# Kernel optimization log

Hardware: AMD Instinct MI355X
Metric: run time of the kernel (lower is better)

The kernel has to match this reference:

```python
import jax, jax.numpy as jnp
import numpy as np
from jax import lax

GAMMA = 1.0
BIG = 1e8  # matches the torch init value 100000000.0


def setup_inputs() -> dict:
    key = jax.random.key(0)
    k1, k2 = jax.random.split(key)
    B, n, m, d = 256, 256, 256, 32
    x = jax.random.normal(k1, (B, n, d), dtype=jnp.float32)
    y = jax.random.normal(k2, (B, m, d), dtype=jnp.float32)
    return {"x": x, "y": y}


def _soft_dtw(x, y, gamma):
    B, n, d = x.shape
    m = y.shape[1]
    # squared euclidean distances, (B, n, m); GEMM form avoids the (B,n,m,d) blowup
    x2 = jnp.sum(x * x, axis=-1)
    y2 = jnp.sum(y * y, axis=-1)
    dist = x2[:, :, None] + y2[:, None, :] - 2.0 * jnp.einsum('bnd,bmd->bnm', x, y)
    dist = jnp.maximum(dist, 0.0)  # cdist(p=2)**2 is nonnegative

    def softmin3(a, b, c):
        s = jnp.stack([a, b, c], axis=0)
        return -gamma * jax.nn.logsumexp(-s / gamma, axis=0)

    big_col = jnp.full((B,), BIG, dtype=x.dtype)

    def row_step(prev_row, d_row):
        # prev_row: (B, m+1) = D[i-1, :];  d_row: (B, m) = dist[:, i-1, :]
        def col_step(cur, inp):
            # cur: (B,) = D[i, j-1]; inp: (dist[i-1,j-1], D[i-1,j], D[i-1,j-1])
            dij, up, diag = inp
            new = dij + softmin3(up, cur, diag)
            return new, new
        xs = (d_row.T, prev_row[:, 1:].T, prev_row[:, :-1].T)  # each (m, B)
        _, vals = lax.scan(col_step, big_col, xs)  # vals: (m, B)
        new_row = jnp.concatenate([big_col[:, None], vals.T], axis=1)  # (B, m+1)
        return new_row, None

    init_row = jnp.concatenate(
        [jnp.zeros((B, 1), x.dtype), jnp.full((B, m), BIG, dtype=x.dtype)], axis=1)
    final_row, _ = lax.scan(row_step, init_row, jnp.swapaxes(dist, 0, 1))  # scan over n rows
    return jnp.mean(final_row[:, m])


def reference(x, y):
    return _soft_dtw(x, y, GAMMA)
```

## Files before the change

### kernel.cpp

```cpp
#include <hip/hip_runtime.h>

#define BIG 1e8f
#define LN2 0.69314718f
#define LOG2E 1.44269504f
#define M2L -2.8853900818f

#define RSLOT 112
#define DRB 1040

#define OFF_XH   116480
#define OFF_X2S  132864
#define OFF_Y2S  133888
#define OFF_RDY  134912
#define OFF_PRG  134976
#define LDS_BYTES 135040

typedef _Float16 half8 __attribute__((ext_vector_type(8)));
typedef _Float16 half2_t __attribute__((ext_vector_type(2)));
typedef float f32x4 __attribute__((ext_vector_type(4)));

__device__ __forceinline__ float exp2g(float x) {
#if __has_builtin(__builtin_amdgcn_exp2f)
    return __builtin_amdgcn_exp2f(x);
#else
    return exp2f(x);
#endif
}
__device__ __forceinline__ float log2g(float x) {
#if __has_builtin(__builtin_amdgcn_logf)
    return __builtin_amdgcn_logf(x);
#else
    return log2f(x);
#endif
}

__device__ __forceinline__ half2_t pkrtz(float a, float b) {
    return __builtin_bit_cast(half2_t, __builtin_amdgcn_cvt_pkrtz(a, b));
}

__device__ __forceinline__ float shfl_up1(float v, float oldv) {
    int r = __builtin_amdgcn_update_dpp(
        __builtin_bit_cast(int, oldv), __builtin_bit_cast(int, v),
        0x138 , 0xf, 0xf, false);
    return __builtin_bit_cast(float, r);
}

__device__ __forceinline__ void dec2(unsigned int w, float& a, float& b) {
    half2_t h = __builtin_bit_cast(half2_t, w);
    a = (float)h[0];
    b = (float)h[1];
}

__device__ __forceinline__ void cell3(float Mu, float Su, float Mg, float Sg,
                                      float Ml, float Sl, float dd,
                                      float& Mo, float& So) {
    const float mu = fminf(fminf(Mu, Mg), Ml);
    const float eu = exp2g(mu - Mu);
    const float eg = exp2g(mu - Mg);
    const float el = exp2g(mu - Ml);
    So = fmaf(Su, eu, fmaf(Sg, eg, Sl * el));
    Mo = dd + mu;
}

#define MASKW0 0x7BFF7BFFu
#define MASKW1 0x70007000u
#define MASKW2 0x60006000u
#define MASKW3 0x50005000u

__global__ __launch_bounds__(128, 1) void sdtw_kernel(
    const float* __restrict__ x, const float* __restrict__ y,
    float* __restrict__ out) {
    extern __shared__ __align__(16) char smem[];
    unsigned char* band = (unsigned char*)smem;
    _Float16* xh = (_Float16*)(smem + OFF_XH);
    float* x2sL = (float*)(smem + OFF_X2S);
    float* y2sL = (float*)(smem + OFF_Y2S);
    volatile int* rdy = (volatile int*)(smem + OFF_RDY);
    volatile int* prg = (volatile int*)(smem + OFF_PRG);

    const int tid = threadIdx.x;
    const int b = blockIdx.x;
    const float* xb = x + (size_t)b * 8192;
    const float* yb = y + (size_t)b * 8192;

#pragma unroll
    for (int rr = 0; rr < 2; rr++) {
        const int r = tid + rr * 128;
        const float4* px = (const float4*)(xb + r * 32);
        union { _Float16 h[32]; half8 v[4]; } uc;
        float s2 = 0.f;
#pragma unroll
        for (int q = 0; q < 8; q++) {
            float4 f = px[q];
            s2 += f.x * f.x + f.y * f.y + f.z * f.z + f.w * f.w;
            uc.h[4 * q + 0] = (_Float16)f.x;
            uc.h[4 * q + 1] = (_Float16)f.y;
            uc.h[4 * q + 2] = (_Float16)f.z;
            uc.h[4 * q + 3] = (_Float16)f.w;
        }
        half8* dst = (half8*)&xh[r * 32];
#pragma unroll
        for (int q = 0; q < 4; q++) dst[q] = uc.v[q];
        x2sL[r] = s2 * LOG2E;

        const float4* py = (const float4*)(yb + r * 32);
        float t2 = 0.f;
#pragma unroll
        for (int q = 0; q < 8; q++) {
            float4 f = py[q];
            t2 += f.x * f.x + f.y * f.y + f.z * f.z + f.w * f.w;
        }
        y2sL[r] = t2 * LOG2E;
    }
    if (tid < 16) rdy[tid] = 0;
    if (tid == 16) *prg = 0;
    __syncthreads();

    if (tid >= 64) {
        const int lane = tid - 64;
        const int qd = lane >> 4, xr = lane & 15;

        half8 yfrag[16];
        float yvL[16];
#pragma unroll
        for (int ci = 0; ci < 16; ci++) {
            const float* yp = yb + (ci * 16 + xr) * 32 + qd * 8;
            float4 f0 = *(const float4*)yp;
            float4 f1 = *(const float4*)(yp + 4);
            half8 v;
            v[0] = (_Float16)f0.x; v[1] = (_Float16)f0.y;
            v[2] = (_Float16)f0.z; v[3] = (_Float16)f0.w;
            v[4] = (_Float16)f1.x; v[5] = (_Float16)f1.y;
            v[6] = (_Float16)f1.z; v[7] = (_Float16)f1.w;
            yfrag[ci] = v;
            yvL[ci] = y2sL[ci * 16 + xr];
        }

        for (int sg = 0; sg < 16; sg++) {
            if (sg >= 6) {
                const int need = 8 * sg - 40;
                while (*prg < need) {}
            }
            const half8 xf = *(const half8*)&xh[(sg * 16 + xr) * 32 + qd * 8];
            const float4 xl = *(const float4*)&x2sL[sg * 16 + qd * 4];
            const int p0 = 8 * sg + 2 * qd;
#pragma unroll
            for (int ci = 0; ci < 16; ci++) {
                f32x4 acc = {0.f, 0.f, 0.f, 0.f};
                acc = __builtin_amdgcn_mfma_f32_16x16x32_f16(xf, yfrag[ci], acc, 0, 0, 0);
                const int c = ci * 16 + xr;
                const float yv = yvL[ci];
                const float d0 = fmaxf(fmaf(M2L, acc[0], xl.x + yv), 0.f);
                const float d1 = fmaxf(fmaf(M2L, acc[1], xl.y + yv), 0.f);
                const float d2 = fmaxf(fmaf(M2L, acc[2], xl.z + yv), 0.f);
                const float d3 = fmaxf(fmaf(M2L, acc[3], xl.w + yv), 0.f);
                const half2_t h01 = pkrtz(d0, d1);
                const half2_t h23 = pkrtz(d2, d3);
                const int dr0 = p0 + (c >> 2);
                int s0_ = dr0;     if (s0_ >= RSLOT) s0_ -= RSLOT;
                int s1_ = dr0 + 1; if (s1_ >= RSLOT) s1_ -= RSLOT;
                *(half2_t*)&band[s0_ * DRB + 4 * c] = h01;
                *(half2_t*)&band[s1_ * DRB + 4 * c] = h23;
            }
            __threadfence_block();
            if (lane == 0) rdy[sg] = 1;
        }
        return;
    }

    const int lane = tid;
    float pBM[4], pBS[4];
    pBM[0] = BIG; pBS[0] = 1.f;
    pBM[1] = BIG; pBS[1] = 1.f;
    pBM[2] = BIG; pBS[2] = 1.f;
    pBM[3] = BIG; pBS[3] = 1.f;
    float G0M = (lane == 0) ? 0.f : BIG, G0S = 1.f;
    float MpA3 = BIG, SpA3 = 1.f, MpB3 = BIG, SpB3 = 1.f;

    float dAc[4], dBc[4];

    auto decode = [&](uint4 w, int s1, bool domask) {
        unsigned wx = w.x, wy = w.y, wz = w.z, ww = w.w;
        if (domask) {
            const bool act = (unsigned)(s1 - 1 - lane) < 128u;
            wx = act ? wx : MASKW0;
            wy = act ? wy : MASKW1;
            wz = act ? wz : MASKW2;
            ww = act ? ww : MASKW3;
        }
        dec2(wx, dAc[0], dBc[0]);
        dec2(wy, dAc[1], dBc[1]);
        dec2(wz, dAc[2], dBc[2]);
        dec2(ww, dAc[3], dBc[3]);
    };

    while (rdy[0] == 0) {}
    decode(*(const uint4*)&band[16 * lane], 1, true);

    auto step = [&](int s_, const char* gb, int koff, bool MASKD) {
        const float MLA = shfl_up1(MpA3, BIG);
        const float MLB = shfl_up1(MpB3, BIG);
        const float SLA = shfl_up1(SpA3, 1.f);
        const float SLB = shfl_up1(SpB3, 1.f);

        const uint4 wnext = *(const uint4*)(gb + koff);

        float MA[4], SA[4];
        cell3(pBM[0], pBS[0], G0M, G0S, MLA, SLA, dAc[0], MA[0], SA[0]);
        cell3(pBM[1], pBS[1], pBM[0], pBS[0], MA[0], SA[0], dAc[1], MA[1], SA[1]);
        cell3(pBM[2], pBS[2], pBM[1], pBS[1], MA[1], SA[1], dAc[2], MA[2], SA[2]);
        cell3(pBM[3], pBS[3], pBM[2], pBS[2], MA[2], SA[2], dAc[3], MA[3], SA[3]);

        float MB[4], SB[4];
        cell3(MA[0], SA[0], MLA, SLA, MLB, SLB, dBc[0], MB[0], SB[0]);
        cell3(MA[1], SA[1], MA[0], SA[0], MB[0], SB[0], dBc[1], MB[1], SB[1]);
        cell3(MA[2], SA[2], MA[1], SA[1], MB[1], SB[1], dBc[2], MB[2], SB[2]);
        cell3(MA[3], SA[3], MA[2], SA[2], MB[2], SB[2], dBc[3], MB[3], SB[3]);

        decode(wnext, s_ + 1, MASKD);

        MpA3 = MA[3]; SpA3 = SA[3];
        MpB3 = MB[3]; SpB3 = SB[3];
#pragma unroll
        for (int k = 0; k < 4; k++) { pBM[k] = MB[k]; pBS[k] = SB[k]; }
        G0M = MLB; G0S = SLB;
    };

    {
        const char* gb0 = (const char*)&band[16 * lane];
#pragma unroll
        for (int s_ = 1; s_ < 8; s_++) step(s_, gb0, s_ * DRB, true);
    }

    for (int g = 1; g < 24; g++) {
        int st = (g > 15) ? 15 : g;
        while (rdy[st] == 0) {}
        if (lane == 0) *prg = 8 * g;
        const int s0 = 8 * g;
        const int slot0 = (s0 >= RSLOT) ? s0 - RSLOT : s0;
        const char* gb = (const char*)&band[slot0 * DRB + 16 * lane];
        if (g >= 8 && g <= 15) {
#pragma unroll
            for (int k = 0; k < 8; k++) step(s0 + k, gb, k * DRB, false);
        } else if (g < 23) {
#pragma unroll
            for (int k = 0; k < 8; k++) step(s0 + k, gb, k * DRB, true);
        } else {
#pragma unroll
            for (int k = 0; k < 8; k++)
                step(s0 + k, gb, (k == 7 ? 6 : k) * DRB, true);
        }
    }

    if (lane == 63)
        atomicAdd(out, (MpB3 - log2g(SpB3)) * (LN2 / 256.f));
}

extern "C" void kernel_launch(void* const* d_in, const int* in_sizes, int n_in,
                              void* d_out, int out_size, void* d_ws, size_t ws_size,
                              hipStream_t stream) {
    const float* x = (const float*)d_in[0];
    const float* y = (const float*)d_in[1];
    float* out = (float*)d_out;
    const int B = in_sizes[0] / (256 * 32);

    (void)hipFuncSetAttribute((const void*)sdtw_kernel,
                              hipFuncAttributeMaxDynamicSharedMemorySize,
                              LDS_BYTES);
    (void)hipMemsetAsync(d_out, 0, sizeof(float), stream);
    sdtw_kernel<<<dim3(B), dim3(128), LDS_BYTES, stream>>>(x, y, out);
}
```

Baseline: 118.7 us.

## Pack two batches per block with smaller LDS ring and finer producer throttling

Each 512-thread block now handles two batch elements, each with its own LDS partition. The band ring buffer shrinks from 112 to 76 slots, and the x fp16 staging is removed: the producer wave loads x rows from global memory with a one-step prefetch. Progress is published at finer granularity so the producer can run closer to the consumer within the smaller ring. Half of the waves exit right after the norm prologue. The aim is to fit more concurrent batches per CU while keeping the MFMA producer and the DP consumer overlapped, at the cost of tighter synchronization and more complex slot wraparound handling (special case at g==9).

```diff
diff --git a/kernel.cpp b/kernel.cpp
--- a/kernel.cpp
+++ b/kernel.cpp
@@ -5,15 +5,15 @@
 #define LOG2E 1.44269504f
 #define M2L -2.8853900818f
 
-#define RSLOT 112
+#define RSLOT 76
 #define DRB 1040
 
-#define OFF_XH   116480
-#define OFF_X2S  132864
-#define OFF_Y2S  133888
-#define OFF_RDY  134912
-#define OFF_PRG  134976
-#define LDS_BYTES 135040
+#define OFF_X2S 79040
+#define OFF_Y2S 80064
+#define OFF_RDY 81088
+#define OFF_PRG 81152
+#define PB      81168
+#define LDS_BYTES (2 * PB)
 
 typedef _Float16 half8 __attribute__((ext_vector_type(8)));
 typedef _Float16 half2_t __attribute__((ext_vector_type(2)));
@@ -67,57 +67,57 @@
 #define MASKW2 0x60006000u
 #define MASKW3 0x50005000u
 
-__global__ __launch_bounds__(128, 1) void sdtw_kernel(
+__global__ __launch_bounds__(512, 2) void sdtw_kernel(
     const float* __restrict__ x, const float* __restrict__ y,
     float* __restrict__ out) {
     extern __shared__ __align__(16) char smem[];
-    unsigned char* band = (unsigned char*)smem;
-    _Float16* xh = (_Float16*)(smem + OFF_XH);
-    float* x2sL = (float*)(smem + OFF_X2S);
-    float* y2sL = (float*)(smem + OFF_Y2S);
-    volatile int* rdy = (volatile int*)(smem + OFF_RDY);
-    volatile int* prg = (volatile int*)(smem + OFF_PRG);
 
     const int tid = threadIdx.x;
-    const int b = blockIdx.x;
-    const float* xb = x + (size_t)b * 8192;
-    const float* yb = y + (size_t)b * 8192;
-
-#pragma unroll
-    for (int rr = 0; rr < 2; rr++) {
-        const int r = tid + rr * 128;
-        const float4* px = (const float4*)(xb + r * 32);
-        union { _Float16 h[32]; half8 v[4]; } uc;
+    const int wid = tid >> 6;
+    const int lane = tid & 63;
+
+    {
+        const int q = tid & 255;
+        const int bq = tid >> 8;
+        const float* xb0 = x + ((size_t)(2 * blockIdx.x + bq)) * 8192;
+        const float* yb0 = y + ((size_t)(2 * blockIdx.x + bq)) * 8192;
+        char* base0 = smem + bq * PB;
+        float* x2s0 = (float*)(base0 + OFF_X2S);
+        float* y2s0 = (float*)(base0 + OFF_Y2S);
+        const float4* px = (const float4*)(xb0 + q * 32);
         float s2 = 0.f;
 #pragma unroll
-        for (int q = 0; q < 8; q++) {
-            float4 f = px[q];
+        for (int k = 0; k < 8; k++) {
+            float4 f = px[k];
             s2 += f.x * f.x + f.y * f.y + f.z * f.z + f.w * f.w;
-            uc.h[4 * q + 0] = (_Float16)f.x;
-            uc.h[4 * q + 1] = (_Float16)f.y;
-            uc.h[4 * q + 2] = (_Float16)f.z;
-            uc.h[4 * q + 3] = (_Float16)f.w;
-        }
-        half8* dst = (half8*)&xh[r * 32];
-#pragma unroll
-        for (int q = 0; q < 4; q++) dst[q] = uc.v[q];
-        x2sL[r] = s2 * LOG2E;
-
-        const float4* py = (const float4*)(yb + r * 32);
+        }
+        x2s0[q] = s2 * LOG2E;
+        const float4* py = (const float4*)(yb0 + q * 32);
         float t2 = 0.f;
 #pragma unroll
-        for (int q = 0; q < 8; q++) {
-            float4 f = py[q];
+        for (int k = 0; k < 8; k++) {
+            float4 f = py[k];
             t2 += f.x * f.x + f.y * f.y + f.z * f.z + f.w * f.w;
         }
-        y2sL[r] = t2 * LOG2E;
+        y2s0[q] = t2 * LOG2E;
+        if (q < 16) ((volatile int*)(base0 + OFF_RDY))[q] = 0;
+        if (q == 16) *(volatile int*)(base0 + OFF_PRG) = 0;
     }
-    if (tid < 16) rdy[tid] = 0;
-    if (tid == 16) *prg = 0;
     __syncthreads();
 
-    if (tid >= 64) {
-        const int lane = tid - 64;
+    if (wid == 2 || wid == 3 || wid == 6 || wid == 7) return;
+
+    const int bi = (wid >= 4) ? 1 : 0;
+    char* base = smem + bi * PB;
+    unsigned char* band = (unsigned char*)base;
+    float* x2sL = (float*)(base + OFF_X2S);
+    float* y2sL = (float*)(base + OFF_Y2S);
+    volatile int* rdy = (volatile int*)(base + OFF_RDY);
+    volatile int* prg = (volatile int*)(base + OFF_PRG);
+    const float* xb = x + ((size_t)(2 * blockIdx.x + bi)) * 8192;
+    const float* yb = y + ((size_t)(2 * blockIdx.x + bi)) * 8192;
+
+    if (wid == 1 || wid == 5) {
         const int qd = lane >> 4, xr = lane & 15;
 
         half8 yfrag[16];
@@ -135,19 +135,37 @@
             yfrag[ci] = v;
             yvL[ci] = y2sL[ci * 16 + xr];
         }
+        half8 xcur;
+        {
+            const float* xp = xb + xr * 32 + qd * 8;
+            float4 f0 = *(const float4*)xp;
+            float4 f1 = *(const float4*)(xp + 4);
+            half8 v;
+            v[0] = (_Float16)f0.x; v[1] = (_Float16)f0.y;
+            v[2] = (_Float16)f0.z; v[3] = (_Float16)f0.w;
+            v[4] = (_Float16)f1.x; v[5] = (_Float16)f1.y;
+            v[6] = (_Float16)f1.z; v[7] = (_Float16)f1.w;
+            xcur = v;
+        }
 
         for (int sg = 0; sg < 16; sg++) {
-            if (sg >= 6) {
-                const int need = 8 * sg - 40;
+            if (sg >= 1) {
+                const int need = 8 * sg - 6;
                 while (*prg < need) {}
             }
-            const half8 xf = *(const half8*)&xh[(sg * 16 + xr) * 32 + qd * 8];
+            float4 nf0, nf1;
+            const bool pf = (sg < 15);
+            if (pf) {
+                const float* xp = xb + ((sg + 1) * 16 + xr) * 32 + qd * 8;
+                nf0 = *(const float4*)xp;
+                nf1 = *(const float4*)(xp + 4);
+            }
             const float4 xl = *(const float4*)&x2sL[sg * 16 + qd * 4];
             const int p0 = 8 * sg + 2 * qd;
 #pragma unroll
             for (int ci = 0; ci < 16; ci++) {
                 f32x4 acc = {0.f, 0.f, 0.f, 0.f};
-                acc = __builtin_amdgcn_mfma_f32_16x16x32_f16(xf, yfrag[ci], acc, 0, 0, 0);
+                acc = __builtin_amdgcn_mfma_f32_16x16x32_f16(xcur, yfrag[ci], acc, 0, 0, 0);
                 const int c = ci * 16 + xr;
                 const float yv = yvL[ci];
                 const float d0 = fmaxf(fmaf(M2L, acc[0], xl.x + yv), 0.f);
@@ -157,18 +175,29 @@
                 const half2_t h01 = pkrtz(d0, d1);
                 const half2_t h23 = pkrtz(d2, d3);
                 const int dr0 = p0 + (c >> 2);
-                int s0_ = dr0;     if (s0_ >= RSLOT) s0_ -= RSLOT;
-                int s1_ = dr0 + 1; if (s1_ >= RSLOT) s1_ -= RSLOT;
+                int s0_ = dr0;
+                if (s0_ >= RSLOT) s0_ -= RSLOT;
+                if (s0_ >= RSLOT) s0_ -= RSLOT;
+                int s1_ = dr0 + 1;
+                if (s1_ >= RSLOT) s1_ -= RSLOT;
+                if (s1_ >= RSLOT) s1_ -= RSLOT;
                 *(half2_t*)&band[s0_ * DRB + 4 * c] = h01;
                 *(half2_t*)&band[s1_ * DRB + 4 * c] = h23;
             }
             __threadfence_block();
             if (lane == 0) rdy[sg] = 1;
+            if (pf) {
+                half8 v;
+                v[0] = (_Float16)nf0.x; v[1] = (_Float16)nf0.y;
+                v[2] = (_Float16)nf0.z; v[3] = (_Float16)nf0.w;
+                v[4] = (_Float16)nf1.x; v[5] = (_Float16)nf1.y;
+                v[6] = (_Float16)nf1.z; v[7] = (_Float16)nf1.w;
+                xcur = v;
+            }
         }
         return;
     }
 
-    const int lane = tid;
     float pBM[4], pBS[4];
     pBM[0] = BIG; pBS[0] = 1.f;
     pBM[1] = BIG; pBS[1] = 1.f;
@@ -228,27 +257,51 @@
 
     {
         const char* gb0 = (const char*)&band[16 * lane];
-#pragma unroll
-        for (int s_ = 1; s_ < 8; s_++) step(s_, gb0, s_ * DRB, true);
+        step(1, gb0, 1 * DRB, true);
+        step(2, gb0, 2 * DRB, true);
+        if (lane == 0) *prg = 2;
+        step(3, gb0, 3 * DRB, true);
+        step(4, gb0, 4 * DRB, true);
+        step(5, gb0, 5 * DRB, true);
+        step(6, gb0, 6 * DRB, true);
+        if (lane == 0) *prg = 6;
+        step(7, gb0, 7 * DRB, true);
     }
 
+    int slot0 = 0;
     for (int g = 1; g < 24; g++) {
+        slot0 += 8;
+        if (slot0 >= RSLOT) slot0 -= RSLOT;
         int st = (g > 15) ? 15 : g;
         while (rdy[st] == 0) {}
-        if (lane == 0) *prg = 8 * g;
         const int s0 = 8 * g;
-        const int slot0 = (s0 >= RSLOT) ? s0 - RSLOT : s0;
         const char* gb = (const char*)&band[slot0 * DRB + 16 * lane];
-        if (g >= 8 && g <= 15) {
-#pragma unroll
-            for (int k = 0; k < 8; k++) step(s0 + k, gb, k * DRB, false);
+        if (g == 9) {
+            const char* gba = (const char*)&band[16 * lane];
+#pragma unroll
+            for (int k = 0; k < 8; k++) {
+                const int sl = (k < 4) ? (72 + k) : (k - 4);
+                step(s0 + k, gba, sl * DRB, false);
+                if (k == 2 || k == 6) { if (lane == 0) *prg = s0 + k; }
+            }
+        } else if (g >= 8 && g <= 15) {
+#pragma unroll
+            for (int k = 0; k < 8; k++) {
+                step(s0 + k, gb, k * DRB, false);
+                if (k == 2 || k == 6) { if (lane == 0) *prg = s0 + k; }
+            }
         } else if (g < 23) {
 #pragma unroll
-            for (int k = 0; k < 8; k++) step(s0 + k, gb, k * DRB, true);
+            for (int k = 0; k < 8; k++) {
+                step(s0 + k, gb, k * DRB, true);
+                if (k == 2 || k == 6) { if (lane == 0) *prg = s0 + k; }
+            }
         } else {
 #pragma unroll
-            for (int k = 0; k < 8; k++)
+            for (int k = 0; k < 8; k++) {
                 step(s0 + k, gb, (k == 7 ? 6 : k) * DRB, true);
+                if (k == 2 || k == 6) { if (lane == 0) *prg = s0 + k; }
+            }
         }
     }
 
@@ -268,5 +321,5 @@
                               hipFuncAttributeMaxDynamicSharedMemorySize,
                               LDS_BYTES);
     (void)hipMemsetAsync(d_out, 0, sizeof(float), stream);
-    sdtw_kernel<<<dim3(B), dim3(128), LDS_BYTES, stream>>>(x, y, out);
-}
+    sdtw_kernel<<<dim3(B / 2), dim3(512), LDS_BYTES, stream>>>(x, y, out);
+}
```

Result: slower. 163.6 us (+37.8%).
